# Optimization experiments

Measured on AMD Instinct MI355X. Metric: run time of the kernel, lower is better.

The kernel has to match this reference:

```python
import jax, jax.numpy as jnp
import numpy as np

B, P, D, H, BOS, C = 64, 8, 1024, 16, 16, 14
S = BOS + C
L, V, HID = 4, 1024, 2048
DH = D // H
TAU, UW = 1.0, 0.1
SOS_IDX, EOS_IDX = 0, 1


def setup_inputs():
    ks = jax.random.split(jax.random.key(0), 16)
    w = lambda k, s: 0.02 * jax.random.normal(k, s, dtype=jnp.float32)
    return {
        "prototypes": jax.random.normal(ks[0], (B, P, D), jnp.float32),
        "query": jax.random.normal(ks[1], (BOS, D), jnp.float32),
        "ca_wq": w(ks[2], (D, D)), "ca_wk": w(ks[3], (D, D)),
        "ca_wv": w(ks[4], (D, D)), "ca_wo": w(ks[5], (D, D)),
        "ln1_w": jnp.ones((L, D)), "ln1_b": jnp.zeros((L, D)),
        "qkv_w": w(ks[6], (L, D, 3 * D)),
        "attn_out_w": w(ks[7], (L, D, D)),
        "rel_bias": w(ks[8], (L, 2 * S - 1, H)),
        "ln2_w": jnp.ones((L, D)), "ln2_b": jnp.zeros((L, D)),
        "mlp_w1": w(ks[9], (L, D, 2 * HID)),
        "mlp_w2": w(ks[10], (L, HID, D)),
        "lnf_w": jnp.ones((D,)), "lnf_b": jnp.zeros((D,)),
        "vocab_w": w(ks[11], (D, V)), "vocab_b": jnp.zeros((V,)),
        "pos_emb": w(ks[12], (C, D)),
        "tok_emb": w(ks[13], (V, D)),
    }


def _ln(x, w, b):
    m = jnp.mean(x, -1, keepdims=True)
    v = jnp.mean(jnp.square(x - m), -1, keepdims=True)
    return (x - m) * jax.lax.rsqrt(v + 1e-5) * w + b


def _forward(prototypes, query, ca_wq, ca_wk, ca_wv, ca_wo, ln1_w, ln1_b, qkv_w,
             attn_out_w, rel_bias, ln2_w, ln2_b, mlp_w1, mlp_w2, lnf_w, lnf_b,
             vocab_w, vocab_b, pos_emb, tok_emb):
    # cross attention (scaling='d' -> divide by head dim) builds the BOS tokens
    qh = (query @ ca_wq).reshape(BOS, H, DH)                 # shared across batch
    kh = (prototypes @ ca_wk).reshape(B, P, H, DH)
    vh = (prototypes @ ca_wv).reshape(B, P, H, DH)
    att = jax.nn.softmax(jnp.einsum('qhd,bkhd->bhqk', qh, kh) / DH, axis=-1)
    bos = jnp.einsum('bhqk,bkhd->bqhd', att, vh).reshape(B, BOS, D) @ ca_wo

    # learned relative position bias -> (L, H, S, S); causal mask (bidirectional=False)
    ridx = jnp.arange(S)[:, None] - jnp.arange(S)[None, :] + (S - 1)
    bias = jnp.transpose(rel_bias[:, ridx], (0, 3, 1, 2))
    causal = jnp.tril(jnp.ones((S, S), dtype=bool))

    def transformer(x):  # pre-LN encoder, SwiGLU MLP (mlp_ratio=2), eval mode
        for l in range(L):
            h = _ln(x, ln1_w[l], ln1_b[l])
            qkv = (h @ qkv_w[l]).reshape(B, S, 3, H, DH)
            sc = jnp.einsum('bqhd,bkhd->bhqk', qkv[:, :, 0], qkv[:, :, 1]) * (DH ** -0.5) + bias[l]
            a = jax.nn.softmax(jnp.where(causal, sc, -1e30), axis=-1)
            x = x + jnp.einsum('bhqk,bkhd->bqhd', a, qkv[:, :, 2]).reshape(B, S, D) @ attn_out_w[l]
            h = _ln(x, ln2_w[l], ln2_b[l])
            u1, u2 = jnp.split(h @ mlp_w1[l], 2, axis=-1)
            x = x + (jax.nn.silu(u1) * u2) @ mlp_w2[l]
        return _ln(x, lnf_w, lnf_b)

    pos_b = jnp.broadcast_to(pos_emb[None], (B, C, D))
    gkey = jax.random.key(42)

    def step(carry, i):
        spoken, _ = carry
        # slots < i hold embedded spoken tokens, slots >= i hold position embeddings
        mask = (jnp.arange(C) < i)[None, :, None]
        x = jnp.concatenate([bos, jnp.where(mask, spoken, pos_b)], axis=1)
        logits = transformer(x)[:, BOS:, :] @ vocab_w + vocab_b
        g = jax.random.gumbel(jax.random.fold_in(gkey, i), logits.shape, logits.dtype)
        soft = jax.nn.softmax((logits + g) / TAU, axis=-1)
        soft = (1.0 - UW) * soft + UW / V
        hard = jax.nn.one_hot(jnp.argmax(soft, axis=-1), V, dtype=soft.dtype)
        st = hard - jax.lax.stop_gradient(soft) + soft  # straight-through one-hot
        return (st @ tok_emb, st), None

    init = (jnp.zeros((B, C, D), jnp.float32), jnp.zeros((B, C, V), jnp.float32))
    (_, st_last), _ = jax.lax.scan(step, init, jnp.arange(C))
    sos = jnp.zeros((B, 1, V), jnp.float32).at[:, 0, SOS_IDX].set(1.0)
    eos = jnp.zeros((B, 1, V), jnp.float32).at[:, 0, EOS_IDX].set(1.0)
    return jnp.concatenate([sos, st_last, eos], axis=1)


def reference(prototypes, query, ca_wq, ca_wk, ca_wv, ca_wo, ln1_w, ln1_b, qkv_w,
              attn_out_w, rel_bias, ln2_w, ln2_b, mlp_w1, mlp_w2, lnf_w, lnf_b,
              vocab_w, vocab_b, pos_emb, tok_emb):
    return _forward(prototypes, query, ca_wq, ca_wk, ca_wv, ca_wo, ln1_w, ln1_b,
                    qkv_w, attn_out_w, rel_bias, ln2_w, ln2_b, mlp_w1, mlp_w2,
                    lnf_w, lnf_b, vocab_w, vocab_b, pos_emb, tok_emb)
```

## Files before the change

### kernel.cpp

```cpp
#include <hip/hip_runtime.h>
#include <stdint.h>
#include <stddef.h>
#include <math.h>

#define NB   64
#define NP   8
#define ND   1024
#define NH   16
#define NBOS 16
#define NC   14
#define NS   30
#define NL   4
#define NV   1024
#define NHID 2048
#define NDH  64

#define JAX_PARTITIONABLE 1

typedef _Float16 half_t;
typedef _Float16 h4_t __attribute__((ext_vector_type(4)));
typedef _Float16 h8_t __attribute__((ext_vector_type(8)));
typedef float f32x4 __attribute__((ext_vector_type(4)));

__device__ __forceinline__ uint32_t rotl32(uint32_t x, int d) {
  return (x << d) | (x >> (32 - d));
}

__device__ __forceinline__ void threefry2x32(uint32_t k0, uint32_t k1,
                                             uint32_t x0, uint32_t x1,
                                             uint32_t& o0, uint32_t& o1) {
  uint32_t ks2 = k0 ^ k1 ^ 0x1BD11BDAu;
  x0 += k0; x1 += k1;
#define TF_R4(a,b,c,d) \
  x0 += x1; x1 = rotl32(x1,(a)); x1 ^= x0; \
  x0 += x1; x1 = rotl32(x1,(b)); x1 ^= x0; \
  x0 += x1; x1 = rotl32(x1,(c)); x1 ^= x0; \
  x0 += x1; x1 = rotl32(x1,(d)); x1 ^= x0;
  TF_R4(13,15,26,6)  x0 += k1;  x1 += ks2 + 1u;
  TF_R4(17,29,16,24) x0 += ks2; x1 += k0 + 2u;
  TF_R4(13,15,26,6)  x0 += k0;  x1 += k1 + 3u;
  TF_R4(17,29,16,24) x0 += k1;  x1 += ks2 + 4u;
  TF_R4(13,15,26,6)  x0 += ks2; x1 += k0 + 5u;
#undef TF_R4
  o0 = x0; o1 = x1;
}

__global__ __launch_bounds__(256) void k_gemm(
    const float* __restrict__ A, const float* __restrict__ Bm,
    float* __restrict__ Cm, const float* __restrict__ bias,
    int M, int N, int K, int epi) {
  __shared__ __align__(16) float As[16][64];
  __shared__ __align__(16) float Bs[16][64];
  const int tid = threadIdx.x;
  const int tx = tid & 15, ty = tid >> 4;
  const int m0 = blockIdx.y * 64, n0 = blockIdx.x * 64;
  const int lar = tid >> 2, lak = (tid & 3) << 2;
  const int lbk = tid >> 4, lbn = (tid & 15) << 2;
  float acc[4][4] = {};
  for (int kt = 0; kt < K; kt += 16) {
    float4 av = make_float4(0.f, 0.f, 0.f, 0.f);
    if (m0 + lar < M)
      av = *(const float4*)(A + (size_t)(m0 + lar) * K + kt + lak);
    float4 bv4 = make_float4(0.f, 0.f, 0.f, 0.f);
    if (n0 + lbn < N)
      bv4 = *(const float4*)(Bm + (size_t)(kt + lbk) * N + n0 + lbn);
    __syncthreads();
    As[lak + 0][lar] = av.x; As[lak + 1][lar] = av.y;
    As[lak + 2][lar] = av.z; As[lak + 3][lar] = av.w;
    *(float4*)(&Bs[lbk][lbn]) = bv4;
    __syncthreads();
#pragma unroll
    for (int kk = 0; kk < 16; ++kk) {
      float4 a4 = *(const float4*)(&As[kk][ty << 2]);
      float4 b4 = *(const float4*)(&Bs[kk][tx << 2]);
      float ar[4] = {a4.x, a4.y, a4.z, a4.w};
      float br[4] = {b4.x, b4.y, b4.z, b4.w};
#pragma unroll
      for (int i2 = 0; i2 < 4; ++i2)
#pragma unroll
        for (int j2 = 0; j2 < 4; ++j2)
          acc[i2][j2] = fmaf(ar[i2], br[j2], acc[i2][j2]);
    }
  }
#pragma unroll
  for (int i2 = 0; i2 < 4; ++i2) {
    int r = m0 + (ty << 2) + i2;
    if (r >= M) continue;
#pragma unroll
    for (int j2 = 0; j2 < 4; ++j2) {
      int c = n0 + (tx << 2) + j2;
      if (c >= N) continue;
      size_t off = (size_t)r * N + c;
      float val = acc[i2][j2];
      if (epi == 1) val += Cm[off];
      else if (epi == 2) val += bias[c];
      Cm[off] = val;
    }
  }
}

__device__ __forceinline__ void gload16(const void* g, const void* l) {
  __builtin_amdgcn_global_load_lds((const __attribute__((address_space(1))) void*)g,
                                   (__attribute__((address_space(3))) void*)l, 16, 0, 0);
}

__device__ __forceinline__ void xcd_swz(int gx, int gy, int& bx, int& by) {
  const int flat = blockIdx.y * gx + blockIdx.x;
  const int chunk = (gx * gy) >> 3;
  const int myid = (flat & 7) * chunk + (flat >> 3);
  bx = myid / gy;
  by = myid % gy;
}

template<int EPI>
__global__ __launch_bounds__(512) void k_g3(
    const half_t* __restrict__ Ah, const half_t* __restrict__ Al,
    const half_t* __restrict__ Bh, const half_t* __restrict__ Bl,
    float* __restrict__ Cout, half_t* __restrict__ Mh, half_t* __restrict__ Ml,
    int M, int N, int K, int CH) {
  __shared__ __align__(16) half_t sAh[2][4096];
  __shared__ __align__(16) half_t sAl[2][4096];
  __shared__ __align__(16) half_t sBh[2][4096];
  __shared__ __align__(16) half_t sBl[2][4096];
  int bx, by; xcd_swz(gridDim.x, gridDim.y, bx, by);
  const int tid = threadIdx.x;
  const int lane = tid & 63, w = tid >> 6;
  const int wm = w >> 2, wn = w & 3;
  const int m0 = by * 128, n0 = bx * 128;
  const int fr = lane & 15, fq = lane >> 4;
  const int kbeg = blockIdx.z * CH;
  const int kend = (kbeg + CH < K) ? (kbeg + CH) : K;
  f32x4 acc[4][2] = {};
  const int r0 = tid >> 2, ch = (tid & 3) * 8;
  const size_t aB = (size_t)(m0 + r0) * K + ch;
  const size_t bB = (size_t)(n0 + r0) * K + ch;
  const int wb = w * 1024;

  auto STAGE = [&](int buf, int kt) {
    gload16(Ah + aB + kt, (char*)(&sAh[buf][0]) + wb);
    gload16(Al + aB + kt, (char*)(&sAl[buf][0]) + wb);
    gload16(Bh + bB + kt, (char*)(&sBh[buf][0]) + wb);
    gload16(Bl + bB + kt, (char*)(&sBl[buf][0]) + wb);
  };

  STAGE(0, kbeg);
  int cur = 0;
  for (int kt = kbeg; kt < kend; kt += 32) {
    const bool has_next = (kt + 32 < kend);
    if (has_next) {
      STAGE(cur ^ 1, kt + 32);
      asm volatile("s_waitcnt vmcnt(4)" ::: "memory");
    } else {
      asm volatile("s_waitcnt vmcnt(0)" ::: "memory");
    }
    asm volatile("s_barrier" ::: "memory");
    const half_t* bAh = &sAh[cur][0] + (wm * 64 + fr) * 32 + fq * 8;
    const half_t* bAl = &sAl[cur][0] + (wm * 64 + fr) * 32 + fq * 8;
    const half_t* bBh = &sBh[cur][0] + (wn * 32 + fr) * 32 + fq * 8;
    const half_t* bBl = &sBl[cur][0] + (wn * 32 + fr) * 32 + fq * 8;
    h8_t a[4], b[2], t[2];
#pragma unroll
    for (int mi = 0; mi < 4; ++mi) a[mi] = *(const h8_t*)(bAh + mi * 512);
#pragma unroll
    for (int ni = 0; ni < 2; ++ni) b[ni] = *(const h8_t*)(bBh + ni * 512);
#pragma unroll
    for (int mi = 0; mi < 4; ++mi)
#pragma unroll
      for (int ni = 0; ni < 2; ++ni)
        acc[mi][ni] = __builtin_amdgcn_mfma_f32_16x16x32_f16(a[mi], b[ni], acc[mi][ni], 0, 0, 0);
#pragma unroll
    for (int ni = 0; ni < 2; ++ni) t[ni] = *(const h8_t*)(bBl + ni * 512);
#pragma unroll
    for (int mi = 0; mi < 4; ++mi)
#pragma unroll
      for (int ni = 0; ni < 2; ++ni)
        acc[mi][ni] = __builtin_amdgcn_mfma_f32_16x16x32_f16(a[mi], t[ni], acc[mi][ni], 0, 0, 0);
#pragma unroll
    for (int mi = 0; mi < 4; ++mi) a[mi] = *(const h8_t*)(bAl + mi * 512);
    asm volatile("s_barrier" ::: "memory");
#pragma unroll
    for (int mi = 0; mi < 4; ++mi)
#pragma unroll
      for (int ni = 0; ni < 2; ++ni)
        acc[mi][ni] = __builtin_amdgcn_mfma_f32_16x16x32_f16(a[mi], b[ni], acc[mi][ni], 0, 0, 0);
    cur ^= 1;
  }
  const float sc = 1.0f / 1024.0f;
  if (EPI == 0) {
    float* Cz = Cout + (size_t)blockIdx.z * M * N;
#pragma unroll
    for (int mi = 0; mi < 4; ++mi) {
      const int row = m0 + wm * 64 + mi * 16 + fq * 4;
#pragma unroll
      for (int ni = 0; ni < 2; ++ni) {
        const int col = n0 + wn * 32 + ni * 16 + fr;
        float* cp = Cz + (size_t)row * N + col;
#pragma unroll
        for (int j = 0; j < 4; ++j) cp[(size_t)j * N] = acc[mi][ni][j] * sc;
      }
    }
  } else if (EPI == 1) {
    const int hid = ((n0 + wn * 32) >> 1) + fr;
#pragma unroll
    for (int mi = 0; mi < 4; ++mi) {
      const int row = m0 + wm * 64 + mi * 16 + fq * 4;
#pragma unroll
      for (int j = 0; j < 4; ++j) {
        const float u1 = acc[mi][0][j] * sc;
        const float u2 = acc[mi][1][j] * sc;
        const float s = 1.0f / (1.0f + expf(-u1));
        const float y = (u1 * s) * u2 * 16.0f;
        const half_t hv = (half_t)y;
        const size_t off = (size_t)(row + j) * NHID + hid;
        Mh[off] = hv;
        Ml[off] = (half_t)(y - (float)hv);
      }
    }
  } else {
#pragma unroll
    for (int mi = 0; mi < 4; ++mi) {
      const int row = m0 + wm * 64 + mi * 16 + fq * 4;
#pragma unroll
      for (int ni = 0; ni < 2; ++ni) {
        const int col = n0 + wn * 32 + ni * 16 + fr;
#pragma unroll
        for (int j = 0; j < 4; ++j) {
          const float v = acc[mi][ni][j] * sc;
          const half_t hv = (half_t)v;
          const size_t off = (size_t)(row + j) * N + col;
          Mh[off] = hv;
          Ml[off] = (half_t)(v - (float)hv);
        }
      }
    }
  }
}

__global__ __launch_bounds__(256) void k_splitw(
    const float* __restrict__ W, half_t* __restrict__ Th, half_t* __restrict__ Tl,
    int K, int N) {
  __shared__ float t[32][33];
  const int kb = blockIdx.x * 32, nb = blockIdx.y * 32;
  const int tid = threadIdx.x;
  const int rr = tid >> 5, cc = tid & 31;
#pragma unroll
  for (int i = 0; i < 4; ++i)
    t[rr + i * 8][cc] = W[(size_t)(kb + rr + i * 8) * N + nb + cc];
  __syncthreads();
#pragma unroll
  for (int i = 0; i < 4; ++i) {
    const int nr = rr + i * 8;
    const float x = t[cc][nr] * 64.0f;
    const half_t h = (half_t)x;
    const float r = x - (float)h;
    const size_t off = (size_t)(nb + nr) * K + kb + cc;
    Th[off] = h;
    Tl[off] = (half_t)r;
  }
}

__global__ __launch_bounds__(256) void k_splitw_swz(
    const float* __restrict__ W, half_t* __restrict__ Th, half_t* __restrict__ Tl,
    int K, int N) {
  __shared__ float t[32][33];
  const int kb = blockIdx.x * 32, nb = blockIdx.y * 32;
  const int tid = threadIdx.x;
  const int rr = tid >> 5, cc = tid & 31;
#pragma unroll
  for (int i = 0; i < 4; ++i)
    t[rr + i * 8][cc] = W[(size_t)(kb + rr + i * 8) * N + nb + cc];
  __syncthreads();
#pragma unroll
  for (int i = 0; i < 4; ++i) {
    const int n = nb + rr + i * 8;
    const int hid = n & (NHID - 1), half = n >> 11;
    const int p = ((hid >> 4) << 5) + (half << 4) + (hid & 15);
    const float x = t[cc][rr + i * 8] * 64.0f;
    const half_t h = (half_t)x;
    const float r = x - (float)h;
    const size_t off = (size_t)p * K + kb + cc;
    Th[off] = h;
    Tl[off] = (half_t)r;
  }
}

__global__ __launch_bounds__(256) void k_ca_attn(
    const float* __restrict__ qh, const float* __restrict__ kh,
    const float* __restrict__ vh, float* __restrict__ bosw) {
  const int b = blockIdx.x >> 4, h = blockIdx.x & 15;
  __shared__ float q[NBOS][NDH], kk[NP][NDH], vv[NP][NDH], a[NBOS][NP];
  const int tid = threadIdx.x;
  for (int idx = tid; idx < NBOS * NDH; idx += 256) {
    int qi = idx >> 6, d = idx & 63;
    q[qi][d] = qh[(size_t)qi * ND + h * NDH + d];
  }
  for (int idx = tid; idx < NP * NDH; idx += 256) {
    int p = idx >> 6, d = idx & 63;
    kk[p][d] = kh[(size_t)(b * NP + p) * ND + h * NDH + d];
    vv[p][d] = vh[(size_t)(b * NP + p) * ND + h * NDH + d];
  }
  __syncthreads();
  if (tid < NBOS * NP) {
    int qi = tid >> 3, p = tid & 7;
    float dot = 0.f;
    for (int d = 0; d < NDH; ++d) dot = fmaf(q[qi][d], kk[p][d], dot);
    a[qi][p] = dot / 64.0f;
  }
  __syncthreads();
  if (tid < NBOS) {
    float mx = a[tid][0];
    for (int p = 1; p < NP; ++p) mx = fmaxf(mx, a[tid][p]);
    float sum = 0.f;
    for (int p = 0; p < NP; ++p) { float e = expf(a[tid][p] - mx); a[tid][p] = e; sum += e; }
    for (int p = 0; p < NP; ++p) a[tid][p] /= sum;
  }
  __syncthreads();
  for (int idx = tid; idx < NBOS * NDH; idx += 256) {
    int qi = idx >> 6, d = idx & 63;
    float o = 0.f;
    for (int p = 0; p < NP; ++p) o = fmaf(a[qi][p], vv[p][d], o);
    bosw[(size_t)(b * NBOS + qi) * ND + h * NDH + d] = o;
  }
}

__global__ __launch_bounds__(256) void k_attn(
    const float* __restrict__ qkv, const float* __restrict__ relb,
    float* __restrict__ attout) {
  const int b = blockIdx.x >> 4, h = blockIdx.x & 15;
  __shared__ float q[NS][NDH], kk[NS][NDH], vv[NS][NDH];
  __shared__ float a[NS][NS];
  const int tid = threadIdx.x;
  for (int idx = tid; idx < NS * NDH; idx += 256) {
    int s = idx >> 6, d = idx & 63;
    size_t base = ((size_t)(b * NS + s) * 3) * ND + h * NDH + d;
    q[s][d]  = qkv[base];
    kk[s][d] = qkv[base + ND];
    vv[s][d] = qkv[base + 2 * ND];
  }
  __syncthreads();
  for (int idx = tid; idx < NS * NS; idx += 256) {
    int i = idx / NS, j = idx % NS;
    float sc = 0.f;
    if (j <= i) {
      float dot = 0.f;
      for (int d = 0; d < NDH; ++d) dot = fmaf(q[i][d], kk[j][d], dot);
      sc = dot * 0.125f + relb[(size_t)(i - j + NS - 1) * NH + h];
    }
    a[i][j] = sc;
  }
  __syncthreads();
  if (tid < NS) {
    const int i = tid;
    float mx = -INFINITY;
    for (int j = 0; j <= i; ++j) mx = fmaxf(mx, a[i][j]);
    float sum = 0.f;
    for (int j = 0; j <= i; ++j) { float e = expf(a[i][j] - mx); a[i][j] = e; sum += e; }
    for (int j = 0; j <= i; ++j) a[i][j] /= sum;
    for (int j = i + 1; j < NS; ++j) a[i][j] = 0.f;
  }
  __syncthreads();
  for (int idx = tid; idx < NS * NDH; idx += 256) {
    int i = idx >> 6, d = idx & 63;
    float o = 0.f;
    for (int j = 0; j < NS; ++j) o = fmaf(a[i][j], vv[j][d], o);
    attout[(size_t)(b * NS + i) * ND + h * NDH + d] = o;
  }
}

__global__ __launch_bounds__(256) void k_attn16p(
    const half_t* __restrict__ Qh, const half_t* __restrict__ Ql,
    const float* __restrict__ relb,
    half_t* __restrict__ Oh, half_t* __restrict__ Ol, int S) {
  const int b = blockIdx.x >> 4, h = blockIdx.x & 15;
  __shared__ float q[NS][NDH], kk[NS][NDH], vv[NS][NDH];
  __shared__ float a[NS][NS];
  const int tid = threadIdx.x;
  for (int idx = tid; idx < S * NDH; idx += 256) {
    int s = idx >> 6, d = idx & 63;
    size_t base = (size_t)(b * S + s) * 3072 + h * NDH + d;
    q[s][d]  = (float)Qh[base] + (float)Ql[base];
    kk[s][d] = (float)Qh[base + 1024] + (float)Ql[base + 1024];
    vv[s][d] = (float)Qh[base + 2048] + (float)Ql[base + 2048];
  }
  __syncthreads();
  for (int idx = tid; idx < S * S; idx += 256) {
    int i = idx / S, j = idx % S;
    float sc = 0.f;
    if (j <= i) {
      float dot = 0.f;
      for (int d = 0; d < NDH; ++d) dot = fmaf(q[i][d], kk[j][d], dot);
      sc = dot * 0.125f + relb[(size_t)(i - j + NS - 1) * NH + h];
    }
    a[i][j] = sc;
  }
  __syncthreads();
  if (tid < S) {
    const int i = tid;
    float mx = -INFINITY;
    for (int j = 0; j <= i; ++j) mx = fmaxf(mx, a[i][j]);
    float sum = 0.f;
    for (int j = 0; j <= i; ++j) { float e = expf(a[i][j] - mx); a[i][j] = e; sum += e; }
    for (int j = 0; j <= i; ++j) a[i][j] /= sum;
    for (int j = i + 1; j < S; ++j) a[i][j] = 0.f;
  }
  __syncthreads();
  for (int idx = tid; idx < S * NDH; idx += 256) {
    int i = idx >> 6, d = idx & 63;
    float o = 0.f;
    for (int j = 0; j < S; ++j) o = fmaf(a[i][j], vv[j][d], o);
    const float y = o * 16.0f;
    const half_t hv = (half_t)y;
    const size_t off = (size_t)(b * S + i) * ND + h * NDH + d;
    Oh[off] = hv;
    Ol[off] = (half_t)(y - (float)hv);
  }
}

__device__ __forceinline__ float block_sum(float val, float* sbuf) {
  for (int off = 32; off > 0; off >>= 1) val += __shfl_down(val, off, 64);
  const int wid = threadIdx.x >> 6;
  if ((threadIdx.x & 63) == 0) sbuf[wid] = val;
  __syncthreads();
  if (threadIdx.x == 0) sbuf[0] = sbuf[0] + sbuf[1] + sbuf[2] + sbuf[3];
  __syncthreads();
  float r = sbuf[0];
  __syncthreads();
  return r;
}

__device__ __forceinline__ void ln_core_emit16(
    float4 x4, const float* w, const float* bvec, float* sbuf,
    half_t* Oh, half_t* Ol, size_t rowoff, int d0) {
  float mean = block_sum(x4.x + x4.y + x4.z + x4.w, sbuf) * (1.0f / 1024.0f);
  float dx0 = x4.x - mean, dx1 = x4.y - mean, dx2 = x4.z - mean, dx3 = x4.w - mean;
  float var = block_sum(dx0*dx0 + dx1*dx1 + dx2*dx2 + dx3*dx3, sbuf) * (1.0f / 1024.0f);
  float rs = 1.0f / sqrtf(var + 1e-5f);
  float4 w4 = *(const float4*)(w + d0);
  float4 b4 = *(const float4*)(bvec + d0);
  float y0 = (dx0 * rs * w4.x + b4.x) * 16.0f;
  float y1 = (dx1 * rs * w4.y + b4.y) * 16.0f;
  float y2 = (dx2 * rs * w4.z + b4.z) * 16.0f;
  float y3 = (dx3 * rs * w4.w + b4.w) * 16.0f;
  h4_t vh, vl;
  vh.x = (half_t)y0; vl.x = (half_t)(y0 - (float)vh.x);
  vh.y = (half_t)y1; vl.y = (half_t)(y1 - (float)vh.y);
  vh.z = (half_t)y2; vl.z = (half_t)(y2 - (float)vh.z);
  vh.w = (half_t)y3; vl.w = (half_t)(y3 - (float)vh.w);
  *(h4_t*)(Oh + rowoff + d0) = vh;
  *(h4_t*)(Ol + rowoff + d0) = vl;
}

__global__ __launch_bounds__(256) void k_ln(
    const float* __restrict__ in, const float* __restrict__ w,
    const float* __restrict__ bvec, float* __restrict__ out) {
  __shared__ float sbuf[4];
  const size_t row = blockIdx.x;
  const int d0 = threadIdx.x << 2;
  float4 x4 = *(const float4*)(in + row * ND + d0);
  float mean = block_sum(x4.x + x4.y + x4.z + x4.w, sbuf) * (1.0f / 1024.0f);
  float dx0 = x4.x - mean, dx1 = x4.y - mean, dx2 = x4.z - mean, dx3 = x4.w - mean;
  float var = block_sum(dx0*dx0 + dx1*dx1 + dx2*dx2 + dx3*dx3, sbuf) * (1.0f / 1024.0f);
  float rs = 1.0f / sqrtf(var + 1e-5f);
  float4 w4 = *(const float4*)(w + d0);
  float4 b4 = *(const float4*)(bvec + d0);
  float4 o;
  o.x = dx0 * rs * w4.x + b4.x;
  o.y = dx1 * rs * w4.y + b4.y;
  o.z = dx2 * rs * w4.z + b4.z;
  o.w = dx3 * rs * w4.w + b4.w;
  *(float4*)(out + row * ND + d0) = o;
}

template<int WRITEX>
__global__ __launch_bounds__(256) void k_red_ln(
    const float* __restrict__ parts, float* __restrict__ X,
    const float* __restrict__ w, const float* __restrict__ bvec,
    half_t* __restrict__ Oh, half_t* __restrict__ Ol, int Mp) {
  __shared__ float sbuf[4];
  const size_t row = blockIdx.x;
  const int d0 = threadIdx.x << 2;
  const size_t off = row * ND + d0;
  const size_t MN = (size_t)Mp * 1024;
  float4 x4 = *(const float4*)(X + off);
  float4 p0 = *(const float4*)(parts + off);
  float4 p1 = *(const float4*)(parts + MN + off);
  float4 p2 = *(const float4*)(parts + 2 * MN + off);
  x4.x += p0.x + p1.x + p2.x; x4.y += p0.y + p1.y + p2.y;
  x4.z += p0.z + p1.z + p2.z; x4.w += p0.w + p1.w + p2.w;
  if (WRITEX) *(float4*)(X + off) = x4;
  ln_core_emit16(x4, w, bvec, sbuf, Oh, Ol, row * ND, d0);
}

__global__ __launch_bounds__(256) void k_red_lnf(
    const float* __restrict__ parts, const float* __restrict__ X,
    const float* __restrict__ w, const float* __restrict__ bvec,
    half_t* __restrict__ Oh, half_t* __restrict__ Ol, int ncur, int S, int Mp) {
  __shared__ float sbuf[4];
  const int blk = blockIdx.x;
  const int b = blk / ncur, c = blk % ncur;
  const size_t row = (size_t)b * S + NBOS + c;
  const int d0 = threadIdx.x << 2;
  const size_t off = row * ND + d0;
  const size_t MN = (size_t)Mp * 1024;
  float4 x4 = *(const float4*)(X + off);
  float4 p0 = *(const float4*)(parts + off);
  float4 p1 = *(const float4*)(parts + MN + off);
  float4 p2 = *(const float4*)(parts + 2 * MN + off);
  x4.x += p0.x + p1.x + p2.x; x4.y += p0.y + p1.y + p2.y;
  x4.z += p0.z + p1.z + p2.z; x4.w += p0.w + p1.w + p2.w;
  ln_core_emit16(x4, w, bvec, sbuf, Oh, Ol, (size_t)blk * ND, d0);
}

__global__ __launch_bounds__(256) void k_lnf(
    const float* __restrict__ x, const float* __restrict__ w,
    const float* __restrict__ bvec, float* __restrict__ out) {
  __shared__ float sbuf[4];
  const int blk = blockIdx.x;
  const int b = blk / NC, c = blk % NC;
  const size_t row = (size_t)b * NS + NBOS + c;
  const int d0 = threadIdx.x << 2;
  float4 x4 = *(const float4*)(x + row * ND + d0);
  float mean = block_sum(x4.x + x4.y + x4.z + x4.w, sbuf) * (1.0f / 1024.0f);
  float dx0 = x4.x - mean, dx1 = x4.y - mean, dx2 = x4.z - mean, dx3 = x4.w - mean;
  float var = block_sum(dx0*dx0 + dx1*dx1 + dx2*dx2 + dx3*dx3, sbuf) * (1.0f / 1024.0f);
  float rs = 1.0f / sqrtf(var + 1e-5f);
  float4 w4 = *(const float4*)(w + d0);
  float4 b4 = *(const float4*)(bvec + d0);
  float4 o;
  o.x = dx0 * rs * w4.x + b4.x;
  o.y = dx1 * rs * w4.y + b4.y;
  o.z = dx2 * rs * w4.z + b4.z;
  o.w = dx3 * rs * w4.w + b4.w;
  *(float4*)(out + (size_t)blk * ND + d0) = o;
}

__device__ __forceinline__ float4 build_row(
    const float* bos, const float* pos_emb, const float* tok_emb,
    const int* tok, const float* stval, int b, int s, int d0, int step) {
  float4 o;
  if (s < NBOS) {
    o = *(const float4*)(bos + (size_t)(b * NBOS + s) * ND + d0);
  } else {
    int j = s - NBOS;
    if (j < step) {
      float sv = stval[b * NC + j];
      int t = tok[b * NC + j];
      float4 e = *(const float4*)(tok_emb + (size_t)t * ND + d0);
      o.x = sv * e.x; o.y = sv * e.y; o.z = sv * e.z; o.w = sv * e.w;
    } else {
      o = *(const float4*)(pos_emb + (size_t)j * ND + d0);
    }
  }
  return o;
}

__global__ __launch_bounds__(256) void k_build_x(
    const float* __restrict__ bos, const float* __restrict__ pos_emb,
    const float* __restrict__ tok_emb, const int* __restrict__ tok,
    const float* __restrict__ stval, float* __restrict__ x, int step) {
  const int row = blockIdx.x;
  const int b = row / NS, s = row % NS;
  const int d0 = threadIdx.x << 2;
  float4 o = build_row(bos, pos_emb, tok_emb, tok, stval, b, s, d0, step);
  *(float4*)(x + (size_t)row * ND + d0) = o;
}

__global__ __launch_bounds__(256) void k_build_ln(
    const float* __restrict__ bos, const float* __restrict__ pos_emb,
    const float* __restrict__ tok_emb, const int* __restrict__ tok,
    const float* __restrict__ stval, const float* __restrict__ w,
    const float* __restrict__ bvec, float* __restrict__ x,
    half_t* __restrict__ Oh, half_t* __restrict__ Ol, int step, int S) {
  __shared__ float sbuf[4];
  const int row = blockIdx.x;
  const int b = row / S, s = row % S;
  const int d0 = threadIdx.x << 2;
  float4 o = build_row(bos, pos_emb, tok_emb, tok, stval, b, s, d0, step);
  *(float4*)(x + (size_t)row * ND + d0) = o;
  ln_core_emit16(o, w, bvec, sbuf, Oh, Ol, (size_t)row * ND, d0);
}

__global__ __launch_bounds__(256) void k_swiglu(const float* __restrict__ u,
                                                float* __restrict__ m) {
  const size_t idx4 = (size_t)blockIdx.x * 256 + threadIdx.x;
  const size_t row = idx4 >> 9;
  const size_t c0 = (idx4 & 511) << 2;
  const float* ur = u + row * (2 * NHID);
  float4 a4 = *(const float4*)(ur + c0);
  float4 b4 = *(const float4*)(ur + NHID + c0);
  float4 o;
  { float s = 1.0f / (1.0f + expf(-a4.x)); o.x = (a4.x * s) * b4.x; }
  { float s = 1.0f / (1.0f + expf(-a4.y)); o.y = (a4.y * s) * b4.y; }
  { float s = 1.0f / (1.0f + expf(-a4.z)); o.z = (a4.z * s) * b4.z; }
  { float s = 1.0f / (1.0f + expf(-a4.w)); o.w = (a4.w * s) * b4.w; }
  *(float4*)(m + row * NHID + c0) = o;
}

template<int GRED>
__global__ __launch_bounds__(256) void k_gumbel_t(
    const float* __restrict__ logits, const float* __restrict__ vb,
    int* __restrict__ tok, float* __restrict__ stval, float* __restrict__ out,
    int step, int finalstep, int ncur, int Mp) {
  const int blk = blockIdx.x;
  const int b = blk / ncur, c = blk % ncur;
  const int tid = threadIdx.x;
  uint32_t fk0, fk1;
  threefry2x32(0u, 42u, 0u, (uint32_t)step, fk0, fk1);
  const float* zrow = logits + (size_t)blk * NV;
  const size_t MN = (size_t)Mp * 1024;
  float y[4];
  float bv = -INFINITY; int bi = 0;
#pragma unroll
  for (int j = 0; j < 4; ++j) {
    const int v = tid + (j << 8);
    const uint32_t idx = (uint32_t)(b * NC + c) * 1024u + (uint32_t)v;
    uint32_t o0, o1, bits;
#if JAX_PARTITIONABLE
    threefry2x32(fk0, fk1, 0u, idx, o0, o1);
    bits = o0 ^ o1;
#else
    const uint32_t half = (uint32_t)(NB * NC * NV / 2);
    uint32_t jj = (idx < half) ? idx : idx - half;
    threefry2x32(fk0, fk1, jj, jj + half, o0, o1);
    bits = (idx < half) ? o0 : o1;
#endif
    float f = __uint_as_float(0x3F800000u | (bits >> 9)) - 1.0f;
    float uu = (f == 0.0f) ? 1.17549435e-38f : f;
    float g = -logf(-logf(uu));
    float z;
    if (GRED) z = zrow[v] + zrow[MN + v] + zrow[2 * MN + v] + vb[v];
    else      z = zrow[v];
    float yv = z + g;
    y[j] = yv;
    if (yv > bv) { bv = yv; bi = v; }
  }
  __shared__ float swv[4]; __shared__ int swi[4];
  __shared__ float s_ymax; __shared__ int s_arg;
  for (int off = 32; off > 0; off >>= 1) {
    float ov = __shfl_down(bv, off, 64);
    int   oi = __shfl_down(bi, off, 64);
    if (ov > bv || (ov == bv && oi < bi)) { bv = ov; bi = oi; }
  }
  if ((tid & 63) == 0) { swv[tid >> 6] = bv; swi[tid >> 6] = bi; }
  __syncthreads();
  if (tid == 0) {
    float mv = swv[0]; int mi = swi[0];
    for (int w2 = 1; w2 < 4; ++w2)
      if (swv[w2] > mv || (swv[w2] == mv && swi[w2] < mi)) { mv = swv[w2]; mi = swi[w2]; }
    s_ymax = mv; s_arg = mi;
  }
  __syncthreads();
  const float ymax = s_ymax;
  float es = 0.f;
#pragma unroll
  for (int j = 0; j < 4; ++j) es += expf(y[j] - ymax);
  __shared__ float sbuf2[4]; __shared__ float s_es;
  for (int off = 32; off > 0; off >>= 1) es += __shfl_down(es, off, 64);
  if ((tid & 63) == 0) sbuf2[tid >> 6] = es;
  __syncthreads();
  if (tid == 0) s_es = sbuf2[0] + sbuf2[1] + sbuf2[2] + sbuf2[3];
  __syncthreads();
  const float esum = s_es;
  const float sprob = 0.9f * (1.0f / esum) + (0.1f / 1024.0f);
  const float stv = (1.0f - sprob) + sprob;
  if (tid == 0) { tok[b * NC + c] = s_arg; stval[b * NC + c] = stv; }
  if (finalstep) {
    float* orow = out + ((size_t)b * (NC + 2) + 1 + c) * NV;
#pragma unroll
    for (int j = 0; j < 4; ++j) {
      const int v = tid + (j << 8);
      orow[v] = (v == s_arg) ? stv : 0.0f;
    }
  }
}

__global__ __launch_bounds__(256) void k_out_init(float* __restrict__ out) {
  const int b = blockIdx.x;
  const int tid = threadIdx.x;
#pragma unroll
  for (int j = 0; j < 4; ++j) {
    const int v = tid + (j << 8);
    out[((size_t)b * (NC + 2) + 0) * NV + v]      = (v == 0) ? 1.0f : 0.0f;
    out[((size_t)b * (NC + 2) + NC + 1) * NV + v] = (v == 1) ? 1.0f : 0.0f;
  }
}

extern "C" void kernel_launch(void* const* d_in, const int* in_sizes, int n_in,
                              void* d_out, int out_size, void* d_ws, size_t ws_size,
                              hipStream_t stream) {
  (void)in_sizes; (void)n_in; (void)out_size;
  const float* prototypes = (const float*)d_in[0];
  const float* query      = (const float*)d_in[1];
  const float* ca_wq      = (const float*)d_in[2];
  const float* ca_wk      = (const float*)d_in[3];
  const float* ca_wv      = (const float*)d_in[4];
  const float* ca_wo      = (const float*)d_in[5];
  const float* ln1_w      = (const float*)d_in[6];
  const float* ln1_b      = (const float*)d_in[7];
  const float* qkv_w      = (const float*)d_in[8];
  const float* attn_out_w = (const float*)d_in[9];
  const float* rel_bias   = (const float*)d_in[10];
  const float* ln2_w      = (const float*)d_in[11];
  const float* ln2_b      = (const float*)d_in[12];
  const float* mlp_w1     = (const float*)d_in[13];
  const float* mlp_w2     = (const float*)d_in[14];
  const float* lnf_w      = (const float*)d_in[15];
  const float* lnf_b      = (const float*)d_in[16];
  const float* vocab_w    = (const float*)d_in[17];
  const float* vocab_b    = (const float*)d_in[18];
  const float* pos_emb    = (const float*)d_in[19];
  const float* tok_emb    = (const float*)d_in[20];
  float* out = (float*)d_out;

  dim3 thr(256);
  dim3 thr512(512);
  const size_t NEED = 234889216ull;

  if (ws_size >= NEED) {
    char* p = (char*)d_ws;
    auto alloc = [&](size_t bytes) { char* r = p; p += (bytes + 255) & ~(size_t)255; return r; };
    half_t *WqH[NL], *WqL[NL], *WaH[NL], *WaL[NL], *W1H[NL], *W1L[NL], *W2H[NL], *W2L[NL];
    for (int l = 0; l < NL; ++l) {
      WqH[l] = (half_t*)alloc(3072 * 1024 * 2);
      WqL[l] = (half_t*)alloc(3072 * 1024 * 2);
      WaH[l] = (half_t*)alloc(1024 * 1024 * 2);
      WaL[l] = (half_t*)alloc(1024 * 1024 * 2);
      W1H[l] = (half_t*)alloc(4096 * 1024 * 2);
      W1L[l] = (half_t*)alloc(4096 * 1024 * 2);
      W2H[l] = (half_t*)alloc(1024 * 2048 * 2);
      W2L[l] = (half_t*)alloc(1024 * 2048 * 2);
    }
    half_t* WvH = (half_t*)alloc(1024 * 1024 * 2);
    half_t* WvL = (half_t*)alloc(1024 * 1024 * 2);
    half_t* Hh  = (half_t*)alloc(1920 * 1024 * 2);
    half_t* Hl  = (half_t*)alloc(1920 * 1024 * 2);
    float* X    = (float*)alloc(1920 * 1024 * 4);
    float* QKV  = (float*)alloc(1920 * 3072 * 4);
    half_t* Mh  = (half_t*)alloc(1920 * 2048 * 2);
    half_t* Ml  = (half_t*)alloc(1920 * 2048 * 2);
    float* LG   = (float*)alloc(896 * 1024 * 4);
    float* BOSb = (float*)alloc(64 * 16 * 1024 * 4);
    float* STV  = (float*)alloc(4096);
    int*   TOK  = (int*)alloc(4096);
    (void)LG;
    float* PARTS = QKV;
    half_t* QKVh = (half_t*)QKV;
    half_t* QKVl = QKVh + (size_t)1920 * 3072;

    for (int l = 0; l < NL; ++l) {
      k_splitw<<<dim3(32, 96), thr, 0, stream>>>(qkv_w + (size_t)l * ND * 3 * ND, WqH[l], WqL[l], 1024, 3072);
      k_splitw<<<dim3(32, 32), thr, 0, stream>>>(attn_out_w + (size_t)l * ND * ND, WaH[l], WaL[l], 1024, 1024);
      k_splitw_swz<<<dim3(32, 128), thr, 0, stream>>>(mlp_w1 + (size_t)l * ND * 2 * NHID, W1H[l], W1L[l], 1024, 4096);
      k_splitw<<<dim3(64, 32), thr, 0, stream>>>(mlp_w2 + (size_t)l * NHID * ND, W2H[l], W2L[l], 2048, 1024);
    }
    k_splitw<<<dim3(32, 32), thr, 0, stream>>>(vocab_w, WvH, WvL, 1024, 1024);

    float* QH = QKV;
    float* KH = QKV + 16384;
    float* VH = QKV + 540672;
    float* BOSW = QKV + 1064960;
    k_gemm<<<dim3(16, 1),  thr, 0, stream>>>(query,      ca_wq, QH,   nullptr, NBOS,    ND, ND, 0);
    k_gemm<<<dim3(16, 8),  thr, 0, stream>>>(prototypes, ca_wk, KH,   nullptr, NB * NP, ND, ND, 0);
    k_gemm<<<dim3(16, 8),  thr, 0, stream>>>(prototypes, ca_wv, VH,   nullptr, NB * NP, ND, ND, 0);
    k_ca_attn<<<dim3(NB * NH), thr, 0, stream>>>(QH, KH, VH, BOSW);
    k_gemm<<<dim3(16, 16), thr, 0, stream>>>(BOSW, ca_wo, BOSb, nullptr, NB * NBOS, ND, ND, 0);
    k_out_init<<<dim3(NB), thr, 0, stream>>>(out);

    for (int i = 0; i < NC; ++i) {
      const int S   = NBOS + i + 1;
      const int Mt  = NB * S;
      const int MtP = (Mt + 127) & ~127;
      const int gy  = MtP / 128;
      const int ncur = i + 1;
      const int Mv  = NB * ncur;
      const int MvP = (Mv + 127) & ~127;
      const int gvy = MvP / 128;

      k_build_ln<<<dim3(Mt), thr, 0, stream>>>(BOSb, pos_emb, tok_emb, TOK, STV,
                                               ln1_w, ln1_b, X, Hh, Hl, i, S);
      for (int l = 0; l < NL; ++l) {
        k_g3<2><<<dim3(24, gy, 1), thr512, 0, stream>>>(Hh, Hl, WqH[l], WqL[l], nullptr, QKVh, QKVl,
                                                        MtP, 3072, 1024, 1024);
        k_attn16p<<<dim3(NB * NH), thr, 0, stream>>>(QKVh, QKVl, rel_bias + (size_t)l * (2 * NS - 1) * NH,
                                                     Hh, Hl, S);
        k_g3<0><<<dim3(8, gy, 3), thr512, 0, stream>>>(Hh, Hl, WaH[l], WaL[l], PARTS, nullptr, nullptr,
                                                       MtP, 1024, 1024, 352);
        k_red_ln<1><<<dim3(Mt), thr, 0, stream>>>(PARTS, X, ln2_w + l * ND, ln2_b + l * ND, Hh, Hl, MtP);
        k_g3<1><<<dim3(32, gy, 1), thr512, 0, stream>>>(Hh, Hl, W1H[l], W1L[l], nullptr, Mh, Ml,
                                                        MtP, 4096, 1024, 1024);
        k_g3<0><<<dim3(8, gy, 3), thr512, 0, stream>>>(Mh, Ml, W2H[l], W2L[l], PARTS, nullptr, nullptr,
                                                       MtP, 1024, 2048, 704);
        if (l < NL - 1)
          k_red_ln<1><<<dim3(Mt), thr, 0, stream>>>(PARTS, X, ln1_w + (l + 1) * ND, ln1_b + (l + 1) * ND,
                                                    Hh, Hl, MtP);
      }
      k_red_lnf<<<dim3(NB * ncur), thr, 0, stream>>>(PARTS, X, lnf_w, lnf_b, Hh, Hl, ncur, S, MtP);
      k_g3<0><<<dim3(8, gvy, 3), thr512, 0, stream>>>(Hh, Hl, WvH, WvL, PARTS, nullptr, nullptr,
                                                      MvP, 1024, 1024, 352);
      k_gumbel_t<1><<<dim3(NB * ncur), thr, 0, stream>>>(PARTS, vocab_b, TOK, STV, out, i,
                                                         (i == NC - 1) ? 1 : 0, ncur, MvP);
    }
    return;
  }

  float* ws = (float*)d_ws;
  float* BOSW = ws + 0;
  float* BOSb = ws + 1048576;
  float* QH   = ws + 2097152;
  float* KH   = ws + 2113536;
  float* VH   = ws + 2637824;
  float* X    = ws + 3162112;
  float* Hb   = ws + 5128192;
  float* HL   = Hb;
  float* LG   = Hb + 917504;
  float* QKV  = ws + 7094272;
  float* U    = QKV;
  float* ATT  = ws + 14958592;
  float* Mb   = ATT;
  float* STV  = ws + 18890752;
  int*   TOK  = (int*)(ws + 18891648);

  k_gemm<<<dim3(16, 1),  thr, 0, stream>>>(query,      ca_wq, QH,   nullptr, NBOS,    ND, ND, 0);
  k_gemm<<<dim3(16, 8),  thr, 0, stream>>>(prototypes, ca_wk, KH,   nullptr, NB * NP, ND, ND, 0);
  k_gemm<<<dim3(16, 8),  thr, 0, stream>>>(prototypes, ca_wv, VH,   nullptr, NB * NP, ND, ND, 0);
  k_ca_attn<<<dim3(NB * NH), thr, 0, stream>>>(QH, KH, VH, BOSW);
  k_gemm<<<dim3(16, 16), thr, 0, stream>>>(BOSW, ca_wo, BOSb, nullptr, NB * NBOS, ND, ND, 0);
  k_out_init<<<dim3(NB), thr, 0, stream>>>(out);

  for (int i = 0; i < NC; ++i) {
    k_build_x<<<dim3(NB * NS), thr, 0, stream>>>(BOSb, pos_emb, tok_emb, TOK, STV, X, i);
    for (int l = 0; l < NL; ++l) {
      k_ln<<<dim3(NB * NS), thr, 0, stream>>>(X, ln1_w + l * ND, ln1_b + l * ND, Hb);
      k_gemm<<<dim3(48, 30), thr, 0, stream>>>(Hb, qkv_w + (size_t)l * ND * 3 * ND, QKV,
                                               nullptr, NB * NS, 3 * ND, ND, 0);
      k_attn<<<dim3(NB * NH), thr, 0, stream>>>(QKV, rel_bias + (size_t)l * (2 * NS - 1) * NH, ATT);
      k_gemm<<<dim3(16, 30), thr, 0, stream>>>(ATT, attn_out_w + (size_t)l * ND * ND, X,
                                               nullptr, NB * NS, ND, ND, 1);
      k_ln<<<dim3(NB * NS), thr, 0, stream>>>(X, ln2_w + l * ND, ln2_b + l * ND, Hb);
      k_gemm<<<dim3(64, 30), thr, 0, stream>>>(Hb, mlp_w1 + (size_t)l * ND * 2 * NHID, U,
                                               nullptr, NB * NS, 2 * NHID, ND, 0);
      k_swiglu<<<dim3(3840), thr, 0, stream>>>(U, Mb);
      k_gemm<<<dim3(16, 30), thr, 0, stream>>>(Mb, mlp_w2 + (size_t)l * NHID * ND, X,
                                               nullptr, NB * NS, ND, NHID, 1);
    }
    k_lnf<<<dim3(NB * NC), thr, 0, stream>>>(X, lnf_w, lnf_b, HL);
    k_gemm<<<dim3(16, 14), thr, 0, stream>>>(HL, vocab_w, LG, vocab_b, NB * NC, NV, ND, 2);
    k_gumbel_t<0><<<dim3(NB * NC), thr, 0, stream>>>(LG, nullptr, TOK, STV, out, i,
                                                     (i == NC - 1) ? 1 : 0, NC, 896);
  }
}
```

Before: 10.43 ms.

## Cache BOS-token K/V per layer and run decode steps only on generated tokens

The 16 BOS-token positions do not depend on generated tokens under a causal mask, so they are now run through all layers once and their per-layer K/V is stored in a cache. Each decode step then runs the transformer only on the generated positions, and a new attention kernel reads the cached BOS K/V alongside the fresh K/V. This removes the repeated full-prefix GEMMs across the 14 steps and shrinks M from 64*(16+i+1) rows to 64*(i+1). It adds cache storage and a copy kernel. The BOS outputs must match the old recomputation exactly, which depends on causality and on the relative bias being position-difference only.

```diff
diff --git a/kernel.cpp b/kernel.cpp
--- a/kernel.cpp
+++ b/kernel.cpp
@@ -416,6 +416,79 @@
   }
 }
 
+__global__ __launch_bounds__(256) void k_copy_kv(
+    const half_t* __restrict__ Qh, const half_t* __restrict__ Ql,
+    half_t* __restrict__ Ch, half_t* __restrict__ Cl) {
+  const int row = blockIdx.x;
+  const int c0 = threadIdx.x * 8;
+  const size_t src = (size_t)row * 3072 + 1024 + c0;
+  const size_t dst = (size_t)row * 2048 + c0;
+  *(h8_t*)(Ch + dst) = *(const h8_t*)(Qh + src);
+  *(h8_t*)(Cl + dst) = *(const h8_t*)(Ql + src);
+}
+
+__global__ __launch_bounds__(256) void k_attn16c(
+    const half_t* __restrict__ Qh, const half_t* __restrict__ Ql,
+    const half_t* __restrict__ Ch, const half_t* __restrict__ Cl,
+    const float* __restrict__ relb,
+    half_t* __restrict__ Oh, half_t* __restrict__ Ol, int ncur) {
+  const int b = blockIdx.x >> 4, h = blockIdx.x & 15;
+  const int S = NBOS + ncur;
+  __shared__ float q[NC][NDH], kk[NS][NDH], vv[NS][NDH];
+  __shared__ float a[NC][NS];
+  const int tid = threadIdx.x;
+  for (int idx = tid; idx < ncur * NDH; idx += 256) {
+    int c = idx >> 6, d = idx & 63;
+    size_t base = (size_t)(b * ncur + c) * 3072 + h * NDH + d;
+    q[c][d] = (float)Qh[base] + (float)Ql[base];
+  }
+  for (int idx = tid; idx < S * NDH; idx += 256) {
+    int j = idx >> 6, d = idx & 63;
+    if (j < NBOS) {
+      size_t r = (size_t)(b * NBOS + j) * 2048 + h * NDH + d;
+      kk[j][d] = (float)Ch[r] + (float)Cl[r];
+      vv[j][d] = (float)Ch[r + 1024] + (float)Cl[r + 1024];
+    } else {
+      size_t base = (size_t)(b * ncur + (j - NBOS)) * 3072 + h * NDH + d;
+      kk[j][d] = (float)Qh[base + 1024] + (float)Ql[base + 1024];
+      vv[j][d] = (float)Qh[base + 2048] + (float)Ql[base + 2048];
+    }
+  }
+  __syncthreads();
+  for (int idx = tid; idx < ncur * S; idx += 256) {
+    int c = idx / S, j = idx % S;
+    const int s = NBOS + c;
+    float sc = 0.f;
+    if (j <= s) {
+      float dot = 0.f;
+      for (int d = 0; d < NDH; ++d) dot = fmaf(q[c][d], kk[j][d], dot);
+      sc = dot * 0.125f + relb[(size_t)(s - j + NS - 1) * NH + h];
+    }
+    a[c][j] = sc;
+  }
+  __syncthreads();
+  if (tid < ncur) {
+    const int c = tid, s = NBOS + c;
+    float mx = -INFINITY;
+    for (int j = 0; j <= s; ++j) mx = fmaxf(mx, a[c][j]);
+    float sum = 0.f;
+    for (int j = 0; j <= s; ++j) { float e = expf(a[c][j] - mx); a[c][j] = e; sum += e; }
+    for (int j = 0; j <= s; ++j) a[c][j] /= sum;
+    for (int j = s + 1; j < S; ++j) a[c][j] = 0.f;
+  }
+  __syncthreads();
+  for (int idx = tid; idx < ncur * NDH; idx += 256) {
+    int c = idx >> 6, d = idx & 63;
+    float o = 0.f;
+    for (int j = 0; j < S; ++j) o = fmaf(a[c][j], vv[j][d], o);
+    const float y = o * 16.0f;
+    const half_t hv = (half_t)y;
+    const size_t off = (size_t)(b * ncur + c) * ND + h * NDH + d;
+    Oh[off] = hv;
+    Ol[off] = (half_t)(y - (float)hv);
+  }
+}
+
 __device__ __forceinline__ float block_sum(float val, float* sbuf) {
   for (int off = 32; off > 0; off >>= 1) val += __shfl_down(val, off, 64);
   const int wid = threadIdx.x >> 6;
@@ -489,26 +562,6 @@
   x4.z += p0.z + p1.z + p2.z; x4.w += p0.w + p1.w + p2.w;
   if (WRITEX) *(float4*)(X + off) = x4;
   ln_core_emit16(x4, w, bvec, sbuf, Oh, Ol, row * ND, d0);
-}
-
-__global__ __launch_bounds__(256) void k_red_lnf(
-    const float* __restrict__ parts, const float* __restrict__ X,
-    const float* __restrict__ w, const float* __restrict__ bvec,
-    half_t* __restrict__ Oh, half_t* __restrict__ Ol, int ncur, int S, int Mp) {
-  __shared__ float sbuf[4];
-  const int blk = blockIdx.x;
-  const int b = blk / ncur, c = blk % ncur;
-  const size_t row = (size_t)b * S + NBOS + c;
-  const int d0 = threadIdx.x << 2;
-  const size_t off = row * ND + d0;
-  const size_t MN = (size_t)Mp * 1024;
-  float4 x4 = *(const float4*)(X + off);
-  float4 p0 = *(const float4*)(parts + off);
-  float4 p1 = *(const float4*)(parts + MN + off);
-  float4 p2 = *(const float4*)(parts + 2 * MN + off);
-  x4.x += p0.x + p1.x + p2.x; x4.y += p0.y + p1.y + p2.y;
-  x4.z += p0.z + p1.z + p2.z; x4.w += p0.w + p1.w + p2.w;
-  ln_core_emit16(x4, w, bvec, sbuf, Oh, Ol, (size_t)blk * ND, d0);
 }
 
 __global__ __launch_bounds__(256) void k_lnf(
@@ -576,6 +629,29 @@
   const int b = row / S, s = row % S;
   const int d0 = threadIdx.x << 2;
   float4 o = build_row(bos, pos_emb, tok_emb, tok, stval, b, s, d0, step);
+  *(float4*)(x + (size_t)row * ND + d0) = o;
+  ln_core_emit16(o, w, bvec, sbuf, Oh, Ol, (size_t)row * ND, d0);
+}
+
+__global__ __launch_bounds__(256) void k_build_ln_c(
+    const float* __restrict__ pos_emb, const float* __restrict__ tok_emb,
+    const int* __restrict__ tok, const float* __restrict__ stval,
+    const float* __restrict__ w, const float* __restrict__ bvec,
+    float* __restrict__ x, half_t* __restrict__ Oh, half_t* __restrict__ Ol,
+    int step, int ncur) {
+  __shared__ float sbuf[4];
+  const int row = blockIdx.x;
+  const int b = row / ncur, c = row % ncur;
+  const int d0 = threadIdx.x << 2;
+  float4 o;
+  if (c < step) {
+    float sv = stval[b * NC + c];
+    int t = tok[b * NC + c];
+    float4 e = *(const float4*)(tok_emb + (size_t)t * ND + d0);
+    o.x = sv * e.x; o.y = sv * e.y; o.z = sv * e.z; o.w = sv * e.w;
+  } else {
+    o = *(const float4*)(pos_emb + (size_t)c * ND + d0);
+  }
   *(float4*)(x + (size_t)row * ND + d0) = o;
   ln_core_emit16(o, w, bvec, sbuf, Oh, Ol, (size_t)row * ND, d0);
 }
@@ -732,20 +808,23 @@
     }
     half_t* WvH = (half_t*)alloc(1024 * 1024 * 2);
     half_t* WvL = (half_t*)alloc(1024 * 1024 * 2);
-    half_t* Hh  = (half_t*)alloc(1920 * 1024 * 2);
-    half_t* Hl  = (half_t*)alloc(1920 * 1024 * 2);
-    float* X    = (float*)alloc(1920 * 1024 * 4);
-    float* QKV  = (float*)alloc(1920 * 3072 * 4);
-    half_t* Mh  = (half_t*)alloc(1920 * 2048 * 2);
-    half_t* Ml  = (half_t*)alloc(1920 * 2048 * 2);
-    float* LG   = (float*)alloc(896 * 1024 * 4);
-    float* BOSb = (float*)alloc(64 * 16 * 1024 * 4);
+    half_t *KVh[NL], *KVl[NL];
+    for (int l = 0; l < NL; ++l) {
+      KVh[l] = (half_t*)alloc(1024 * 2048 * 2);
+      KVl[l] = (half_t*)alloc(1024 * 2048 * 2);
+    }
+    half_t* Hh  = (half_t*)alloc(1024 * 1024 * 2);
+    half_t* Hl  = (half_t*)alloc(1024 * 1024 * 2);
+    float*  X   = (float*)alloc(1024 * 1024 * 4);
+    char*  QKVr = alloc(12582912);
+    half_t* Mh  = (half_t*)alloc(1024 * 2048 * 2);
+    half_t* Ml  = (half_t*)alloc(1024 * 2048 * 2);
     float* STV  = (float*)alloc(4096);
     int*   TOK  = (int*)alloc(4096);
-    (void)LG;
-    float* PARTS = QKV;
-    half_t* QKVh = (half_t*)QKV;
-    half_t* QKVl = QKVh + (size_t)1920 * 3072;
+    float* PARTS = (float*)QKVr;
+    half_t* QKVh = (half_t*)QKVr;
+    half_t* QKVl = QKVh + (size_t)1024 * 3072;
+    float* BOSb  = (float*)Mh;
 
     for (int l = 0; l < NL; ++l) {
       k_splitw<<<dim3(32, 96), thr, 0, stream>>>(qkv_w + (size_t)l * ND * 3 * ND, WqH[l], WqL[l], 1024, 3072);
@@ -755,10 +834,10 @@
     }
     k_splitw<<<dim3(32, 32), thr, 0, stream>>>(vocab_w, WvH, WvL, 1024, 1024);
 
-    float* QH = QKV;
-    float* KH = QKV + 16384;
-    float* VH = QKV + 540672;
-    float* BOSW = QKV + 1064960;
+    float* QH = (float*)QKVr;
+    float* KH = (float*)QKVr + 16384;
+    float* VH = (float*)QKVr + 540672;
+    float* BOSW = (float*)QKVr + 1064960;
     k_gemm<<<dim3(16, 1),  thr, 0, stream>>>(query,      ca_wq, QH,   nullptr, NBOS,    ND, ND, 0);
     k_gemm<<<dim3(16, 8),  thr, 0, stream>>>(prototypes, ca_wk, KH,   nullptr, NB * NP, ND, ND, 0);
     k_gemm<<<dim3(16, 8),  thr, 0, stream>>>(prototypes, ca_wv, VH,   nullptr, NB * NP, ND, ND, 0);
@@ -766,39 +845,57 @@
     k_gemm<<<dim3(16, 16), thr, 0, stream>>>(BOSW, ca_wo, BOSb, nullptr, NB * NBOS, ND, ND, 0);
     k_out_init<<<dim3(NB), thr, 0, stream>>>(out);
 
+    k_build_ln<<<dim3(1024), thr, 0, stream>>>(BOSb, pos_emb, tok_emb, TOK, STV,
+                                               ln1_w, ln1_b, X, Hh, Hl, 0, NBOS);
+    for (int l = 0; l < NL; ++l) {
+      k_g3<2><<<dim3(24, 8, 1), thr512, 0, stream>>>(Hh, Hl, WqH[l], WqL[l], nullptr, QKVh, QKVl,
+                                                     1024, 3072, 1024, 1024);
+      k_copy_kv<<<dim3(1024), thr, 0, stream>>>(QKVh, QKVl, KVh[l], KVl[l]);
+      k_attn16p<<<dim3(NB * NH), thr, 0, stream>>>(QKVh, QKVl, rel_bias + (size_t)l * (2 * NS - 1) * NH,
+                                                   Hh, Hl, NBOS);
+      k_g3<0><<<dim3(8, 8, 3), thr512, 0, stream>>>(Hh, Hl, WaH[l], WaL[l], PARTS, nullptr, nullptr,
+                                                    1024, 1024, 1024, 352);
+      k_red_ln<1><<<dim3(1024), thr, 0, stream>>>(PARTS, X, ln2_w + l * ND, ln2_b + l * ND, Hh, Hl, 1024);
+      k_g3<1><<<dim3(32, 8, 1), thr512, 0, stream>>>(Hh, Hl, W1H[l], W1L[l], nullptr, Mh, Ml,
+                                                     1024, 4096, 1024, 1024);
+      k_g3<0><<<dim3(8, 8, 3), thr512, 0, stream>>>(Mh, Ml, W2H[l], W2L[l], PARTS, nullptr, nullptr,
+                                                    1024, 1024, 2048, 704);
+      if (l < NL - 1)
+        k_red_ln<1><<<dim3(1024), thr, 0, stream>>>(PARTS, X, ln1_w + (l + 1) * ND, ln1_b + (l + 1) * ND,
+                                                    Hh, Hl, 1024);
+    }
+
     for (int i = 0; i < NC; ++i) {
-      const int S   = NBOS + i + 1;
-      const int Mt  = NB * S;
-      const int MtP = (Mt + 127) & ~127;
-      const int gy  = MtP / 128;
       const int ncur = i + 1;
-      const int Mv  = NB * ncur;
-      const int MvP = (Mv + 127) & ~127;
-      const int gvy = MvP / 128;
-
-      k_build_ln<<<dim3(Mt), thr, 0, stream>>>(BOSb, pos_emb, tok_emb, TOK, STV,
-                                               ln1_w, ln1_b, X, Hh, Hl, i, S);
+      const int Mv = NB * ncur;
+      const int MP = (Mv + 127) & ~127;
+      const int gy = MP / 128;
+
+      k_build_ln_c<<<dim3(Mv), thr, 0, stream>>>(pos_emb, tok_emb, TOK, STV,
+                                                 ln1_w, ln1_b, X, Hh, Hl, i, ncur);
       for (int l = 0; l < NL; ++l) {
         k_g3<2><<<dim3(24, gy, 1), thr512, 0, stream>>>(Hh, Hl, WqH[l], WqL[l], nullptr, QKVh, QKVl,
-                                                        MtP, 3072, 1024, 1024);
-        k_attn16p<<<dim3(NB * NH), thr, 0, stream>>>(QKVh, QKVl, rel_bias + (size_t)l * (2 * NS - 1) * NH,
-                                                     Hh, Hl, S);
+                                                        MP, 3072, 1024, 1024);
+        k_attn16c<<<dim3(NB * NH), thr, 0, stream>>>(QKVh, QKVl, KVh[l], KVl[l],
+                                                     rel_bias + (size_t)l * (2 * NS - 1) * NH,
+                                                     Hh, Hl, ncur);
         k_g3<0><<<dim3(8, gy, 3), thr512, 0, stream>>>(Hh, Hl, WaH[l], WaL[l], PARTS, nullptr, nullptr,
-                                                       MtP, 1024, 1024, 352);
-        k_red_ln<1><<<dim3(Mt), thr, 0, stream>>>(PARTS, X, ln2_w + l * ND, ln2_b + l * ND, Hh, Hl, MtP);
+                                                       MP, 1024, 1024, 352);
+        k_red_ln<1><<<dim3(Mv), thr, 0, stream>>>(PARTS, X, ln2_w + l * ND, ln2_b + l * ND, Hh, Hl, MP);
         k_g3<1><<<dim3(32, gy, 1), thr512, 0, stream>>>(Hh, Hl, W1H[l], W1L[l], nullptr, Mh, Ml,
-                                                        MtP, 4096, 1024, 1024);
+                                                        MP, 4096, 1024, 1024);
         k_g3<0><<<dim3(8, gy, 3), thr512, 0, stream>>>(Mh, Ml, W2H[l], W2L[l], PARTS, nullptr, nullptr,
-                                                       MtP, 1024, 2048, 704);
+                                                       MP, 1024, 2048, 704);
         if (l < NL - 1)
-          k_red_ln<1><<<dim3(Mt), thr, 0, stream>>>(PARTS, X, ln1_w + (l + 1) * ND, ln1_b + (l + 1) * ND,
-                                                    Hh, Hl, MtP);
+          k_red_ln<1><<<dim3(Mv), thr, 0, stream>>>(PARTS, X, ln1_w + (l + 1) * ND, ln1_b + (l + 1) * ND,
+                                                    Hh, Hl, MP);
+        else
+          k_red_ln<0><<<dim3(Mv), thr, 0, stream>>>(PARTS, X, lnf_w, lnf_b, Hh, Hl, MP);
       }
-      k_red_lnf<<<dim3(NB * ncur), thr, 0, stream>>>(PARTS, X, lnf_w, lnf_b, Hh, Hl, ncur, S, MtP);
-      k_g3<0><<<dim3(8, gvy, 3), thr512, 0, stream>>>(Hh, Hl, WvH, WvL, PARTS, nullptr, nullptr,
-                                                      MvP, 1024, 1024, 352);
-      k_gumbel_t<1><<<dim3(NB * ncur), thr, 0, stream>>>(PARTS, vocab_b, TOK, STV, out, i,
-                                                         (i == NC - 1) ? 1 : 0, ncur, MvP);
+      k_g3<0><<<dim3(8, gy, 3), thr512, 0, stream>>>(Hh, Hl, WvH, WvL, PARTS, nullptr, nullptr,
+                                                     MP, 1024, 1024, 352);
+      k_gumbel_t<1><<<dim3(Mv), thr, 0, stream>>>(PARTS, vocab_b, TOK, STV, out, i,
+                                                  (i == NC - 1) ? 1 : 0, ncur, MP);
     }
     return;
   }
```

Result: faster. 8.853 ms (-15.1%).
